# Kernel tuning notes

Measured on AMD Instinct MI355X. Metric: run time of the kernel, lower is better.

## Reference

```python
import jax, jax.numpy as jnp
import numpy as np

N_HEAD = 16

def setup_inputs() -> dict:
    key = jax.random.key(0)
    k1, k2, k3 = jax.random.split(key, 3)
    B, T, C = 4, 2048, 1024
    x = jax.random.normal(k1, (B, T, C), dtype=jnp.float32)
    Wqkv = jax.random.normal(k2, (C, 3 * C), dtype=jnp.float32) * (C ** -0.5)
    bqkv = jnp.zeros((3 * C,), dtype=jnp.float32)
    Wout = jax.random.normal(k3, (C, C), dtype=jnp.float32) * (C ** -0.5)
    bout = jnp.zeros((C,), dtype=jnp.float32)
    return {"x": x, "Wqkv": Wqkv, "bqkv": bqkv, "Wout": Wout, "bout": bout}

def reference(x, Wqkv, bqkv, Wout, bout):
    B, T, C = x.shape
    H = N_HEAD
    hd = C // H
    scale = hd ** -0.5
    qkv = x @ Wqkv + bqkv                      # [B,T,3C]
    q, k, v = jnp.split(qkv, 3, axis=-1)
    # [B,T,C] -> [B,H,T,hd]
    q = q.reshape(B, T, H, hd).transpose(0, 2, 1, 3)
    k = k.reshape(B, T, H, hd).transpose(0, 2, 1, 3)
    v = v.reshape(B, T, H, hd).transpose(0, 2, 1, 3)
    attn = jnp.einsum('bhqd,bhkd->bhqk', q, k) * scale  # [B,H,T,T]
    mask = jnp.tril(jnp.ones((T, T), dtype=bool))
    attn = jnp.where(mask[None, None], attn, -jnp.inf)
    attn = jax.nn.softmax(attn, axis=-1)       # dropout p=0.0 -> identity
    out = jnp.einsum('bhqk,bhkd->bhqd', attn, v)
    out = out.transpose(0, 2, 1, 3).reshape(B, T, C)
    out = out @ Wout + bout
    return (out, k, v)
```

## Files before the change

kernel.cpp:

```cpp
#include <hip/hip_runtime.h>
#include <stdint.h>

typedef short bf16x8 __attribute__((ext_vector_type(8)));
typedef float f32x4 __attribute__((ext_vector_type(4)));

#define MFMA16(A, B, C) __builtin_amdgcn_mfma_f32_16x16x32_bf16((A), (B), (C), 0, 0, 0)

__device__ inline unsigned short f2bf(float x) {
    unsigned int b = __builtin_bit_cast(unsigned int, x);
    b += 0x7fffu + ((b >> 16) & 1u);
    return (unsigned short)(b >> 16);
}
__device__ inline unsigned pack2bf(float x, float y) {
    unsigned a = __builtin_bit_cast(unsigned, x) + 0x8000u;
    unsigned b = __builtin_bit_cast(unsigned, y) + 0x8000u;
    return __builtin_amdgcn_perm(b, a, 0x07060302u);
}

#if __has_builtin(__builtin_amdgcn_exp2f)
#define EXP2(x) __builtin_amdgcn_exp2f(x)
#else
__device__ inline float fast_exp2_(float x) {
    float r;
    asm("v_exp_f32 %0, %1" : "=v"(r) : "v"(x));
    return r;
}
#define EXP2(x) fast_exp2_(x)
#endif

typedef __attribute__((address_space(1))) const void glob_cv;
typedef __attribute__((address_space(3))) void lds_v;
__device__ __forceinline__ void async_copy16(void* lds, const void* g) {
    __builtin_amdgcn_global_load_lds((glob_cv*)g, (lds_v*)lds, 16, 0, 0);
}

__global__ __launch_bounds__(256) void cast_bf16_kernel(const float* __restrict__ in,
                                                        unsigned short* __restrict__ out) {
    size_t g = (size_t)blockIdx.x * 256 + threadIdx.x;
    float4 a = ((const float4*)in)[g * 2 + 0];
    float4 b = ((const float4*)in)[g * 2 + 1];
    union { unsigned short u[8]; uint4 v; } r;
    r.u[0] = f2bf(a.x); r.u[1] = f2bf(a.y); r.u[2] = f2bf(a.z); r.u[3] = f2bf(a.w);
    r.u[4] = f2bf(b.x); r.u[5] = f2bf(b.y); r.u[6] = f2bf(b.z); r.u[7] = f2bf(b.w);
    ((uint4*)out)[g] = r.v;
}

__global__ __launch_bounds__(256) void tcast_kernel(const float* __restrict__ in,
                                                    unsigned short* __restrict__ out,
                                                    int R, int C) {
    __shared__ float tile[32][33];
    int tx = threadIdx.x & 31, ty = threadIdx.x >> 5;
    int c0 = blockIdx.x * 32, r0 = blockIdx.y * 32;
#pragma unroll
    for (int i = 0; i < 4; i++)
        tile[ty + i * 8][tx] = in[(size_t)(r0 + ty + i * 8) * C + c0 + tx];
    __syncthreads();
#pragma unroll
    for (int i = 0; i < 4; i++)
        out[(size_t)(c0 + ty + i * 8) * R + r0 + tx] = f2bf(tile[tx][ty + i * 8]);
}

__global__ __launch_bounds__(256) void tv_kernel(const float* __restrict__ in,
                                                 unsigned short* __restrict__ out) {
    __shared__ float tile[32][33];
    int tx = threadIdx.x & 31, ty = threadIdx.x >> 5;
    int d0 = blockIdx.x * 32, t0 = blockIdx.y * 32, bh = blockIdx.z;
    const float* vin = in + (size_t)bh * 2048 * 64;
    unsigned short* vout = out + (size_t)bh * 64 * 2048;
#pragma unroll
    for (int i = 0; i < 4; i++)
        tile[ty + i * 8][tx] = vin[(size_t)(t0 + ty + i * 8) * 64 + d0 + tx];
    __syncthreads();
#pragma unroll
    for (int i = 0; i < 4; i++)
        vout[(size_t)(d0 + ty + i * 8) * 2048 + t0 + tx] = f2bf(tile[tx][ty + i * 8]);
}

template <int MODE>
__global__ __launch_bounds__(256) void gemm_bt_kernel(
    const unsigned short* __restrict__ A, const unsigned short* __restrict__ Bt,
    const float* __restrict__ bias, int K,
    unsigned short* __restrict__ q_out, float* __restrict__ k_out, float* __restrict__ v_out,
    float* __restrict__ c_out) {
    __shared__ __align__(16) unsigned short As[2 * 128 * 32];
    __shared__ __align__(16) unsigned short Bs[2 * 128 * 32];
    int tid = threadIdx.x;
    int w = tid >> 6, l = tid & 63;
    int quad = l >> 4, cl = l & 15;
    int wm = w & 1, wn = w >> 1;
    int m0 = blockIdx.y * 128, n0 = blockIdx.x * 128;

    f32x4 acc[4][4] = {};

    int srow = w * 16 + (l >> 2);
    int scol = (l & 3) * 8;
    const unsigned short* Ap = A + (size_t)(m0 + srow) * K + scol;
    const unsigned short* Bp = Bt + (size_t)(n0 + srow) * K + scol;

    {
        unsigned short* a0 = &As[w * 512];
        unsigned short* b0 = &Bs[w * 512];
        async_copy16(a0, Ap);
        async_copy16(a0 + 2048, Ap + (size_t)64 * K);
        async_copy16(b0, Bp);
        async_copy16(b0 + 2048, Bp + (size_t)64 * K);
    }

    for (int k0 = 0; k0 < K; k0 += 32) {
        int bo = (k0 >> 5) & 1;
        __syncthreads();
        if (k0 + 32 < K) {
            unsigned short* a0 = &As[(bo ^ 1) * 4096 + w * 512];
            unsigned short* b0 = &Bs[(bo ^ 1) * 4096 + w * 512];
            async_copy16(a0, Ap + k0 + 32);
            async_copy16(a0 + 2048, Ap + (size_t)64 * K + k0 + 32);
            async_copy16(b0, Bp + k0 + 32);
            async_copy16(b0 + 2048, Bp + (size_t)64 * K + k0 + 32);
        }
        bf16x8 af[4], bfr[4];
#pragma unroll
        for (int t = 0; t < 4; t++) {
            af[t]  = *(const bf16x8*)&As[bo * 4096 + (wm * 64 + t * 16 + cl) * 32 + quad * 8];
            bfr[t] = *(const bf16x8*)&Bs[bo * 4096 + (wn * 64 + t * 16 + cl) * 32 + quad * 8];
        }
#pragma unroll
        for (int mt = 0; mt < 4; mt++)
#pragma unroll
            for (int nt = 0; nt < 4; nt++)
                acc[mt][nt] = MFMA16(af[mt], bfr[nt], acc[mt][nt]);
    }

    if (MODE == 0) {
#pragma unroll
        for (int mt = 0; mt < 4; mt++)
#pragma unroll
            for (int nt = 0; nt < 4; nt++) {
                int n = n0 + wn * 64 + nt * 16 + cl;
                float bn = bias[n];
                int sec = n >> 10, cc = n & 1023, h = cc >> 6, d = cc & 63;
#pragma unroll
                for (int r = 0; r < 4; r++) {
                    int m = m0 + wm * 64 + mt * 16 + quad * 4 + r;
                    int b = m >> 11, t = m & 2047;
                    float val = acc[mt][nt][r] + bn;
                    size_t idx = ((size_t)(b * 16 + h) * 2048 + t) * 64 + d;
                    if (sec == 0)      q_out[idx] = f2bf(val * 0.18033688011112042f);
                    else if (sec == 1) k_out[idx] = val;
                    else               v_out[idx] = val;
                }
            }
    } else {
#pragma unroll
        for (int mt = 0; mt < 4; mt++)
#pragma unroll
            for (int nt = 0; nt < 4; nt++) {
                int n = n0 + wn * 64 + nt * 16 + cl;
                float bn = bias[n];
#pragma unroll
                for (int r = 0; r < 4; r++) {
                    int m = m0 + wm * 64 + mt * 16 + quad * 4 + r;
                    c_out[(size_t)m * 1024 + n] = acc[mt][nt][r] + bn;
                }
            }
    }
}

__global__ __launch_bounds__(256) void attn_kernel(
    const unsigned short* __restrict__ Q,
    const float* __restrict__ Kin,
    const unsigned short* __restrict__ Vt,
    unsigned short* __restrict__ Out) {
    __shared__ __align__(16) unsigned short Ks[2 * 64 * 72];
    __shared__ __align__(16) unsigned short Vts[2 * 64 * 64];
    __shared__ __align__(16) unsigned short Ps[128 * 72];
    int tid = threadIdx.x;
    int w = tid >> 6, l = tid & 63;
    int quad = l >> 4, cl = l & 15;
    int cl7 = cl & 7;
    int bh = blockIdx.x;
    int b = bh >> 4, h = bh & 15;
    int qt = 15 - (int)blockIdx.y;
    int qw0 = qt * 128 + w * 32;
    int nkt = 2 * qt + 2;

    int srow = tid >> 2, sch = tid & 3;
    const float* kbase = Kin + ((size_t)bh * 2048 + srow) * 64 + sch * 16;
    unsigned lK = srow * 72 + sch * 16;
    int vrow = 8 * w + (l >> 3);
    int vchk = (l & 7) ^ (l >> 3);
    const unsigned short* vg = Vt + ((size_t)bh * 64 + vrow) * 2048 + vchk * 8;

    const unsigned short* qb = Q + ((size_t)bh * 2048 + qw0 + cl) * 64;
    bf16x8 qf[2][2];
    qf[0][0] = *(const bf16x8*)(qb + quad * 8);
    qf[0][1] = *(const bf16x8*)(qb + 32 + quad * 8);
    qf[1][0] = *(const bf16x8*)(qb + 16 * 64 + quad * 8);
    qf[1][1] = *(const bf16x8*)(qb + 16 * 64 + 32 + quad * 8);

    f32x4 accO[2][4] = {};
    float lloc[2] = {0.f, 0.f};

    float4 kr0, kr1, kr2, kr3;
    {
        const float4* kpp = (const float4*)kbase;
        kr0 = kpp[0]; kr1 = kpp[1]; kr2 = kpp[2]; kr3 = kpp[3];
    }
    {
        unsigned short* vsb = &Vts[w * 512];
        async_copy16(vsb, vg);
        async_copy16(vsb + 2048, vg + (size_t)32 * 2048);
    }

    for (int kt = 0; kt < nkt; ++kt) {
        unsigned bo = (unsigned)(kt & 1);
        uint4 c0, c1;
        c0.x = pack2bf(kr0.x, kr0.y); c0.y = pack2bf(kr0.z, kr0.w);
        c0.z = pack2bf(kr1.x, kr1.y); c0.w = pack2bf(kr1.z, kr1.w);
        c1.x = pack2bf(kr2.x, kr2.y); c1.y = pack2bf(kr2.z, kr2.w);
        c1.z = pack2bf(kr3.x, kr3.y); c1.w = pack2bf(kr3.z, kr3.w);
        *(uint4*)&Ks[bo * 4608 + lK] = c0;
        *(uint4*)&Ks[bo * 4608 + lK + 8] = c1;
        __syncthreads();

        if (kt + 1 < nkt) {
            const float4* kpp = (const float4*)(kbase + (size_t)(kt + 1) * 4096);
            kr0 = kpp[0]; kr1 = kpp[1]; kr2 = kpp[2]; kr3 = kpp[3];
            unsigned short* vsb = &Vts[(bo ^ 1) * 4096 + w * 512];
            async_copy16(vsb, vg + (size_t)(kt + 1) * 64);
            async_copy16(vsb + 2048, vg + (size_t)32 * 2048 + (size_t)(kt + 1) * 64);
        }
        if (kt * 64 > qw0 + 31) continue;

        f32x4 s[2][4];
        __builtin_amdgcn_s_setprio(1);
#pragma unroll
        for (int mt = 0; mt < 4; mt++) {
            bf16x8 kf0 = *(const bf16x8*)&Ks[bo * 4608 + (mt * 16 + cl) * 72 + quad * 8];
            bf16x8 kf1 = *(const bf16x8*)&Ks[bo * 4608 + (mt * 16 + cl) * 72 + 32 + quad * 8];
#pragma unroll
            for (int ng = 0; ng < 2; ng++) {
                f32x4 a = {};
                a = MFMA16(kf0, qf[ng][0], a);
                a = MFMA16(kf1, qf[ng][1], a);
                s[ng][mt] = a;
            }
        }
        __builtin_amdgcn_s_setprio(0);
        if (kt * 64 + 63 > qw0) {
#pragma unroll
            for (int ng = 0; ng < 2; ng++) {
                int qg = qw0 + ng * 16 + cl;
#pragma unroll
                for (int mt = 0; mt < 4; mt++)
#pragma unroll
                    for (int r = 0; r < 4; r++) {
                        int kv = kt * 64 + mt * 16 + quad * 4 + r;
                        if (kv > qg) s[ng][mt][r] = -1e30f;
                    }
            }
        }
        bf16x8 pf[2][2];
#pragma unroll
        for (int ng = 0; ng < 2; ng++) {
            unsigned pbase = (unsigned)(w * 32 + ng * 16 + cl) * 72;
#pragma unroll
            for (int mt = 0; mt < 4; mt++) {
                float e0 = EXP2(s[ng][mt][0]);
                float e1 = EXP2(s[ng][mt][1]);
                float e2 = EXP2(s[ng][mt][2]);
                float e3 = EXP2(s[ng][mt][3]);
                lloc[ng] += (e0 + e1) + (e2 + e3);
                uint2 pv;
                pv.x = pack2bf(e0, e1);
                pv.y = pack2bf(e2, e3);
                *(uint2*)&Ps[pbase + mt * 16 + quad * 4] = pv;
            }
            pf[ng][0] = *(const bf16x8*)&Ps[pbase + quad * 8];
            pf[ng][1] = *(const bf16x8*)&Ps[pbase + 32 + quad * 8];
        }
        __builtin_amdgcn_s_setprio(1);
#pragma unroll
        for (int mt = 0; mt < 4; mt++) {
            int vr = mt * 16 + cl;
            bf16x8 vf0 = *(const bf16x8*)&Vts[bo * 4096 + vr * 64 + (quad ^ cl7) * 8];
            bf16x8 vf1 = *(const bf16x8*)&Vts[bo * 4096 + vr * 64 + ((quad | 4) ^ cl7) * 8];
#pragma unroll
            for (int ng = 0; ng < 2; ng++) {
                accO[ng][mt] = MFMA16(vf0, pf[ng][0], accO[ng][mt]);
                accO[ng][mt] = MFMA16(vf1, pf[ng][1], accO[ng][mt]);
            }
        }
        __builtin_amdgcn_s_setprio(0);
    }

#pragma unroll
    for (int ng = 0; ng < 2; ng++) {
        float lv = lloc[ng];
        lv += __shfl_xor(lv, 16);
        lv += __shfl_xor(lv, 32);
        float inv = 1.0f / lv;
        size_t obase = ((size_t)(b * 2048 + qw0 + ng * 16 + cl)) * 1024 + h * 64;
#pragma unroll
        for (int mt = 0; mt < 4; mt++) {
            uint2 ov;
            ov.x = (unsigned)f2bf(accO[ng][mt][0] * inv) | ((unsigned)f2bf(accO[ng][mt][1] * inv) << 16);
            ov.y = (unsigned)f2bf(accO[ng][mt][2] * inv) | ((unsigned)f2bf(accO[ng][mt][3] * inv) << 16);
            *(uint2*)&Out[obase + mt * 16 + quad * 4] = ov;
        }
    }
}

extern "C" void kernel_launch(void* const* d_in, const int* in_sizes, int n_in,
                              void* d_out, int out_size, void* d_ws, size_t ws_size,
                              hipStream_t stream) {
    const float* x    = (const float*)d_in[0];
    const float* Wqkv = (const float*)d_in[1];
    const float* bqkv = (const float*)d_in[2];
    const float* Wout = (const float*)d_in[3];
    const float* bout = (const float*)d_in[4];

    float* out   = (float*)d_out;
    float* k_out = out + 8388608;
    float* v_out = out + 16777216;

    char* ws = (char*)d_ws;
    unsigned short* xb    = (unsigned short*)(ws);
    unsigned short* WqkvT = (unsigned short*)(ws + 16777216);
    unsigned short* WoutT = (unsigned short*)(ws + 23068672);
    unsigned short* q_ws  = (unsigned short*)(ws + 25165824);
    unsigned short* vT    = (unsigned short*)(ws + 41943040);
    unsigned short* attn  = xb;

    cast_bf16_kernel<<<4096, 256, 0, stream>>>(x, xb);
    tcast_kernel<<<dim3(96, 32), 256, 0, stream>>>(Wqkv, WqkvT, 1024, 3072);
    tcast_kernel<<<dim3(32, 32), 256, 0, stream>>>(Wout, WoutT, 1024, 1024);
    gemm_bt_kernel<0><<<dim3(24, 64), 256, 0, stream>>>(xb, WqkvT, bqkv, 1024,
                                                        q_ws, k_out, v_out, nullptr);
    tv_kernel<<<dim3(2, 64, 64), 256, 0, stream>>>(v_out, vT);
    attn_kernel<<<dim3(64, 16), 256, 0, stream>>>(q_ws, k_out, vT, attn);
    gemm_bt_kernel<1><<<dim3(8, 64), 256, 0, stream>>>(attn, WoutT, bout, 1024,
                                                       nullptr, nullptr, nullptr, out);
}
```

Before: 304.4 us.

## Replace QKV projection GEMM with 256x256-tile, 512-thread pipelined kernel

Adds a dedicated QKV GEMM kernel that computes 256x256 output tiles with 8 waves. It uses a BK=64 double-buffered LDS pipeline fed by async global-to-LDS copies with an XOR-swizzled layout, plus a block-index swizzle to improve L2 reuse. MFMA groups are interleaved with barriers and s_setprio so loads overlap compute, and the larger tiles raise arithmetic intensity over the previous 128x128 kernel. In exchange it uses more registers and LDS (64KB per block), and the hand-written vmcnt/barrier schedule adds risk of correctness or occupancy problems.

```diff
diff --git a/kernel.cpp b/kernel.cpp
--- a/kernel.cpp
+++ b/kernel.cpp
@@ -33,6 +33,9 @@
 __device__ __forceinline__ void async_copy16(void* lds, const void* g) {
     __builtin_amdgcn_global_load_lds((glob_cv*)g, (lds_v*)lds, 16, 0, 0);
 }
+
+#define FENCE asm volatile("" ::: "memory")
+#define SBAR do { FENCE; __builtin_amdgcn_s_barrier(); FENCE; } while (0)
 
 __global__ __launch_bounds__(256) void cast_bf16_kernel(const float* __restrict__ in,
                                                         unsigned short* __restrict__ out) {
@@ -74,6 +77,140 @@
 #pragma unroll
     for (int i = 0; i < 4; i++)
         vout[(size_t)(d0 + ty + i * 8) * 2048 + t0 + tx] = f2bf(tile[tx][ty + i * 8]);
+}
+
+__global__ __launch_bounds__(512, 2) void qkv_gemm256_kernel(
+    const unsigned short* __restrict__ A, const unsigned short* __restrict__ Bt,
+    const float* __restrict__ bias, int K,
+    unsigned short* __restrict__ q_out, float* __restrict__ k_out, float* __restrict__ v_out) {
+    __shared__ __align__(16) unsigned short As[2 * 16384];
+    __shared__ __align__(16) unsigned short Bs[2 * 16384];
+    const int tid = threadIdx.x;
+    const int w = tid >> 6, l = tid & 63;
+    const int quad = l >> 4, cl = l & 15, cl7 = l & 7;
+    const int wm = w & 1, wn = w >> 1;
+
+    int bid = (int)blockIdx.x;
+    int swz = (bid & 7) * 48 + (bid >> 3);
+    const int m0 = (swz / 12) * 256, n0 = (swz % 12) * 256;
+
+    const int srow = w * 8 + (l >> 3);
+    const int schk = (l & 7) ^ ((l >> 3) & 7);
+    const unsigned short* Ag = A + (size_t)(m0 + srow) * K + schk * 8;
+    const unsigned short* Bg = Bt + (size_t)(n0 + srow) * K + schk * 8;
+    const int ldsw = w * 512;
+
+#define STAGE2(base, Gp, h, tk)                                                              \
+    do {                                                                                     \
+        async_copy16((void*)&(base)[(h) * 8192 + ldsw], (Gp) + (size_t)((h) * 128) * K + (tk));          \
+        async_copy16((void*)&(base)[(h) * 8192 + 4096 + ldsw], (Gp) + (size_t)((h) * 128 + 64) * K + (tk)); \
+    } while (0)
+
+    const unsigned aRdBase = wm * 8192 + cl * 64;
+    const unsigned bRdBase = (wn >> 1) * 8192 + (((wn & 1) * 64) + cl) * 64;
+    const unsigned pk0 = ((quad) ^ cl7) * 8;
+    const unsigned pk1 = ((4 + quad) ^ cl7) * 8;
+
+    f32x4 acc[8][4] = {};
+    bf16x8 bf[4][2];
+
+    STAGE2(As, Ag, 0, 0); STAGE2(As, Ag, 1, 0);
+    STAGE2(Bs, Bg, 0, 0); STAGE2(Bs, Bg, 1, 0);
+
+    const int NT = K >> 6;
+
+#define LD_A(ab_, mt_, pk_) (*(const bf16x8*)&As[(ab_) + aRdBase + (mt_) * 1024 + (pk_)])
+
+#define MFMA_PAIR(ma_, mb_, a0_, a1_, b0_, b1_)                    \
+    do {                                                           \
+        __builtin_amdgcn_s_setprio(1);                             \
+        _Pragma("unroll")                                          \
+        for (int nt = 0; nt < 4; nt++) {                           \
+            acc[ma_][nt] = MFMA16(a0_, bf[nt][0], acc[ma_][nt]);   \
+            acc[ma_][nt] = MFMA16(a1_, bf[nt][1], acc[ma_][nt]);   \
+            acc[mb_][nt] = MFMA16(b0_, bf[nt][0], acc[mb_][nt]);   \
+            acc[mb_][nt] = MFMA16(b1_, bf[nt][1], acc[mb_][nt]);   \
+        }                                                          \
+        __builtin_amdgcn_s_setprio(0);                             \
+    } while (0)
+
+#define TILE(kt_, c_)                                                                     \
+    do {                                                                                  \
+        const int ktn = (kt_) + 1;                                                        \
+        const bool hasN = ktn < NT;                                                       \
+        const unsigned ab = (c_) * 16384;                                                 \
+        const unsigned sb = ((c_) ^ 1) * 16384;                                           \
+                \
+        if (hasN) { STAGE2((&As[sb]), Ag, 0, ktn * 64); STAGE2((&Bs[sb]), Bg, 0, ktn * 64); \
+                    asm volatile("s_waitcnt vmcnt(4)" ::: "memory"); }                    \
+        else      { asm volatile("s_waitcnt vmcnt(0)" ::: "memory"); }                    \
+        SBAR;                                           \
+        _Pragma("unroll")                                                                 \
+        for (int nt = 0; nt < 4; nt++) {                                                  \
+            bf[nt][0] = *(const bf16x8*)&Bs[ab + bRdBase + nt * 1024 + pk0];              \
+            bf[nt][1] = *(const bf16x8*)&Bs[ab + bRdBase + nt * 1024 + pk1];              \
+        }                                                                                 \
+        {                                                                                 \
+            bf16x8 a00 = LD_A(ab, 0, pk0), a01 = LD_A(ab, 0, pk1);                        \
+            bf16x8 a10 = LD_A(ab, 1, pk0), a11 = LD_A(ab, 1, pk1);                        \
+            SBAR;                                                                         \
+            MFMA_PAIR(0, 1, a00, a01, a10, a11);                                          \
+            SBAR;                                                                         \
+        }                                                                                 \
+                                                                             \
+        {                                                                                 \
+            bf16x8 a00 = LD_A(ab, 2, pk0), a01 = LD_A(ab, 2, pk1);                        \
+            bf16x8 a10 = LD_A(ab, 3, pk0), a11 = LD_A(ab, 3, pk1);                        \
+            SBAR;                                                                         \
+            MFMA_PAIR(2, 3, a00, a01, a10, a11);                                          \
+            SBAR;                                                                         \
+        }                                                                                 \
+                                                   \
+        {                                                                                 \
+            if (hasN) { STAGE2((&As[sb]), Ag, 1, ktn * 64); STAGE2((&Bs[sb]), Bg, 1, ktn * 64); } \
+            bf16x8 a00 = LD_A(ab, 4, pk0), a01 = LD_A(ab, 4, pk1);                        \
+            bf16x8 a10 = LD_A(ab, 5, pk0), a11 = LD_A(ab, 5, pk1);                        \
+            SBAR;                                                                         \
+            MFMA_PAIR(4, 5, a00, a01, a10, a11);                                          \
+            SBAR;                                                                         \
+        }                                                                                 \
+                                                                             \
+        {                                                                                 \
+            bf16x8 a00 = LD_A(ab, 6, pk0), a01 = LD_A(ab, 6, pk1);                        \
+            bf16x8 a10 = LD_A(ab, 7, pk0), a11 = LD_A(ab, 7, pk1);                        \
+            SBAR;                                                                         \
+            MFMA_PAIR(6, 7, a00, a01, a10, a11);                                          \
+            SBAR;                                                                         \
+        }                                                                                 \
+    } while (0)
+
+    for (int kt = 0; kt < NT; kt += 2) {
+        TILE(kt, 0);
+        TILE(kt + 1, 1);
+    }
+#undef TILE
+#undef MFMA_PAIR
+#undef LD_A
+#undef STAGE2
+
+#pragma unroll
+    for (int mt = 0; mt < 8; mt++)
+#pragma unroll
+        for (int nt = 0; nt < 4; nt++) {
+            int n = n0 + wn * 64 + nt * 16 + cl;
+            float bn = bias[n];
+            int sec = n >> 10, ccc = n & 1023, h = ccc >> 6, d = ccc & 63;
+#pragma unroll
+            for (int r = 0; r < 4; r++) {
+                int m = m0 + wm * 128 + mt * 16 + quad * 4 + r;
+                int b = m >> 11, t = m & 2047;
+                float val = acc[mt][nt][r] + bn;
+                size_t idx = ((size_t)(b * 16 + h) * 2048 + t) * 64 + d;
+                if (sec == 0)      q_out[idx] = f2bf(val * 0.18033688011112042f);
+                else if (sec == 1) k_out[idx] = val;
+                else               v_out[idx] = val;
+            }
+        }
 }
 
 template <int MODE>
@@ -334,8 +471,8 @@
     cast_bf16_kernel<<<4096, 256, 0, stream>>>(x, xb);
     tcast_kernel<<<dim3(96, 32), 256, 0, stream>>>(Wqkv, WqkvT, 1024, 3072);
     tcast_kernel<<<dim3(32, 32), 256, 0, stream>>>(Wout, WoutT, 1024, 1024);
-    gemm_bt_kernel<0><<<dim3(24, 64), 256, 0, stream>>>(xb, WqkvT, bqkv, 1024,
-                                                        q_ws, k_out, v_out, nullptr);
+    qkv_gemm256_kernel<<<384, 512, 0, stream>>>(xb, WqkvT, bqkv, 1024,
+                                                q_ws, k_out, v_out);
     tv_kernel<<<dim3(2, 64, 64), 256, 0, stream>>>(v_out, vT);
     attn_kernel<<<dim3(64, 16), 256, 0, stream>>>(q_ws, k_out, vT, attn);
     gemm_bt_kernel<1><<<dim3(8, 64), 256, 0, stream>>>(attn, WoutT, bout, 1024,
```

Measured after the change: 313.0 us. +2.8%, slower.

## Replace QKV GEMM with 256x256-tile pipelined kernel and fuse V transpose

Applied to the files above, without the earlier changes.

Adds a dedicated QKV projection GEMM using 256x256 tiles, 512 threads, and XOR-swizzled LDS. Loads are async global-to-LDS and double-buffered, with split-phase prefetch, s_setprio around the MFMA bursts, and a block-index swizzle for L2 locality. The epilogue also writes the bf16 transposed V directly, so the separate tv_kernel launch and its re-read of V disappear. The bigger tiles raise register and LDS pressure, and the vT stores are scattered 8-byte writes.

```diff
diff --git a/kernel.cpp b/kernel.cpp
--- a/kernel.cpp
+++ b/kernel.cpp
@@ -33,6 +33,9 @@
 __device__ __forceinline__ void async_copy16(void* lds, const void* g) {
     __builtin_amdgcn_global_load_lds((glob_cv*)g, (lds_v*)lds, 16, 0, 0);
 }
+
+#define FENCE asm volatile("" ::: "memory")
+#define SBAR do { FENCE; __builtin_amdgcn_s_barrier(); FENCE; } while (0)
 
 __global__ __launch_bounds__(256) void cast_bf16_kernel(const float* __restrict__ in,
                                                         unsigned short* __restrict__ out) {
@@ -60,20 +63,128 @@
         out[(size_t)(c0 + ty + i * 8) * R + r0 + tx] = f2bf(tile[tx][ty + i * 8]);
 }
 
-__global__ __launch_bounds__(256) void tv_kernel(const float* __restrict__ in,
-                                                 unsigned short* __restrict__ out) {
-    __shared__ float tile[32][33];
-    int tx = threadIdx.x & 31, ty = threadIdx.x >> 5;
-    int d0 = blockIdx.x * 32, t0 = blockIdx.y * 32, bh = blockIdx.z;
-    const float* vin = in + (size_t)bh * 2048 * 64;
-    unsigned short* vout = out + (size_t)bh * 64 * 2048;
-#pragma unroll
-    for (int i = 0; i < 4; i++)
-        tile[ty + i * 8][tx] = vin[(size_t)(t0 + ty + i * 8) * 64 + d0 + tx];
-    __syncthreads();
-#pragma unroll
-    for (int i = 0; i < 4; i++)
-        vout[(size_t)(d0 + ty + i * 8) * 2048 + t0 + tx] = f2bf(tile[tx][ty + i * 8]);
+__global__ __launch_bounds__(512, 2) void qkv_gemm256_kernel(
+    const unsigned short* __restrict__ A, const unsigned short* __restrict__ Bt,
+    const float* __restrict__ bias, int K,
+    unsigned short* __restrict__ q_out, float* __restrict__ k_out, float* __restrict__ v_out,
+    unsigned short* __restrict__ vT) {
+    __shared__ __align__(16) unsigned short As[2 * 16384];
+    __shared__ __align__(16) unsigned short Bs[2 * 16384];
+    const int tid = threadIdx.x;
+    const int w = tid >> 6, l = tid & 63;
+    const int quad = l >> 4, cl = l & 15, cl7 = l & 7;
+    const int wm = w & 1, wn = w >> 1;
+
+    int bid = (int)blockIdx.x;
+    int swz = (bid & 7) * 48 + (bid >> 3);
+    const int m0 = (swz / 12) * 256, n0 = (swz % 12) * 256;
+
+    const int srow = w * 8 + (l >> 3);
+    const int schk = (l & 7) ^ ((l >> 3) & 7);
+    const unsigned short* Ag = A + (size_t)(m0 + srow) * K + schk * 8;
+    const unsigned short* Bg = Bt + (size_t)(n0 + srow) * K + schk * 8;
+    const int ldsw = w * 512;
+
+#define STAGE2(base, Gp, h, tk)                                                              \
+    do {                                                                                     \
+        async_copy16((void*)&(base)[(h) * 8192 + ldsw], (Gp) + (size_t)((h) * 128) * K + (tk));          \
+        async_copy16((void*)&(base)[(h) * 8192 + 4096 + ldsw], (Gp) + (size_t)((h) * 128 + 64) * K + (tk)); \
+    } while (0)
+
+    const unsigned aRdBase = wm * 8192 + cl * 64;
+    const unsigned bRdBase = (wn >> 1) * 8192 + (((wn & 1) * 64) + cl) * 64;
+    const unsigned pk0 = ((quad) ^ cl7) * 8;
+    const unsigned pk1 = ((4 + quad) ^ cl7) * 8;
+
+    f32x4 acc[8][4] = {};
+
+    STAGE2(As, Ag, 0, 0); STAGE2(As, Ag, 1, 0);
+    STAGE2(Bs, Bg, 0, 0); STAGE2(Bs, Bg, 1, 0);
+
+    const int NT = K >> 6;
+
+#define PHASE(ab_, h_, nn_, PRE)                                                              \
+    do {                                                                                      \
+        bf16x8 af[4][2], bq[2][2];                                                            \
+        _Pragma("unroll")                                                                     \
+        for (int i = 0; i < 4; i++) {                                                         \
+            af[i][0] = *(const bf16x8*)&As[(ab_) + aRdBase + ((h_) * 4 + i) * 1024 + pk0];    \
+            af[i][1] = *(const bf16x8*)&As[(ab_) + aRdBase + ((h_) * 4 + i) * 1024 + pk1];    \
+        }                                                                                     \
+        _Pragma("unroll")                                                                     \
+        for (int j = 0; j < 2; j++) {                                                         \
+            bq[j][0] = *(const bf16x8*)&Bs[(ab_) + bRdBase + ((nn_) * 2 + j) * 1024 + pk0];   \
+            bq[j][1] = *(const bf16x8*)&Bs[(ab_) + bRdBase + ((nn_) * 2 + j) * 1024 + pk1];   \
+        }                                                                                     \
+        PRE;                                                                                  \
+        SBAR;                                                                                 \
+        __builtin_amdgcn_s_setprio(1);                                                        \
+        _Pragma("unroll")                                                                     \
+        for (int i = 0; i < 4; i++)                                                           \
+            _Pragma("unroll")                                                                 \
+            for (int j = 0; j < 2; j++) {                                                     \
+                acc[(h_) * 4 + i][(nn_) * 2 + j] =                                            \
+                    MFMA16(af[i][0], bq[j][0], acc[(h_) * 4 + i][(nn_) * 2 + j]);             \
+                acc[(h_) * 4 + i][(nn_) * 2 + j] =                                            \
+                    MFMA16(af[i][1], bq[j][1], acc[(h_) * 4 + i][(nn_) * 2 + j]);             \
+            }                                                                                 \
+        __builtin_amdgcn_s_setprio(0);                                                        \
+        SBAR;                                                                                 \
+    } while (0)
+
+#define TILE(kt_, c_)                                                                         \
+    do {                                                                                      \
+        const int ktn = (kt_) + 1;                                                            \
+        const bool hasN = ktn < NT;                                                           \
+        const unsigned ab = (c_) * 16384;                                                     \
+        const unsigned sb = ((c_) ^ 1) * 16384;                                               \
+        if (hasN) { STAGE2((&As[sb]), Ag, 0, ktn * 64); STAGE2((&Bs[sb]), Bg, 0, ktn * 64);   \
+                    asm volatile("s_waitcnt vmcnt(4)" ::: "memory"); }                        \
+        else      { asm volatile("s_waitcnt vmcnt(0)" ::: "memory"); }                        \
+        SBAR;                                                            \
+        PHASE(ab, 0, 0, );                                                                    \
+        PHASE(ab, 1, 0,                                                                       \
+              if (hasN) { STAGE2((&As[sb]), Ag, 1, ktn * 64); STAGE2((&Bs[sb]), Bg, 1, ktn * 64); }); \
+        PHASE(ab, 0, 1, );                                                                    \
+        PHASE(ab, 1, 1, );                                                                    \
+    } while (0)
+
+    for (int kt = 0; kt < NT; kt += 2) {
+        TILE(kt, 0);
+        TILE(kt + 1, 1);
+    }
+#undef TILE
+#undef PHASE
+#undef STAGE2
+
+#pragma unroll
+    for (int mt = 0; mt < 8; mt++)
+#pragma unroll
+        for (int nt = 0; nt < 4; nt++) {
+            int n = n0 + wn * 64 + nt * 16 + cl;
+            float bn = bias[n];
+            int sec = n >> 10, ccc = n & 1023, h = ccc >> 6, d = ccc & 63;
+            int mb = m0 + wm * 128 + mt * 16 + quad * 4;
+            int b = mb >> 11, t = mb & 2047;
+            size_t idx0 = ((size_t)(b * 16 + h) * 2048 + t) * 64 + d;
+            if (sec == 0) {
+#pragma unroll
+                for (int r = 0; r < 4; r++)
+                    q_out[idx0 + (size_t)r * 64] = f2bf((acc[mt][nt][r] + bn) * 0.18033688011112042f);
+            } else if (sec == 1) {
+#pragma unroll
+                for (int r = 0; r < 4; r++)
+                    k_out[idx0 + (size_t)r * 64] = acc[mt][nt][r] + bn;
+            } else {
+#pragma unroll
+                for (int r = 0; r < 4; r++)
+                    v_out[idx0 + (size_t)r * 64] = acc[mt][nt][r] + bn;
+                uint2 vv;
+                vv.x = pack2bf(acc[mt][nt][0] + bn, acc[mt][nt][1] + bn);
+                vv.y = pack2bf(acc[mt][nt][2] + bn, acc[mt][nt][3] + bn);
+                *(uint2*)&vT[((size_t)(b * 16 + h) * 64 + d) * 2048 + t] = vv;
+            }
+        }
 }
 
 template <int MODE>
@@ -334,9 +445,8 @@
     cast_bf16_kernel<<<4096, 256, 0, stream>>>(x, xb);
     tcast_kernel<<<dim3(96, 32), 256, 0, stream>>>(Wqkv, WqkvT, 1024, 3072);
     tcast_kernel<<<dim3(32, 32), 256, 0, stream>>>(Wout, WoutT, 1024, 1024);
-    gemm_bt_kernel<0><<<dim3(24, 64), 256, 0, stream>>>(xb, WqkvT, bqkv, 1024,
-                                                        q_ws, k_out, v_out, nullptr);
-    tv_kernel<<<dim3(2, 64, 64), 256, 0, stream>>>(v_out, vT);
+    qkv_gemm256_kernel<<<384, 512, 0, stream>>>(xb, WqkvT, bqkv, 1024,
+                                                q_ws, k_out, v_out, vT);
     attn_kernel<<<dim3(64, 16), 256, 0, stream>>>(q_ws, k_out, vT, attn);
     gemm_bt_kernel<1><<<dim3(8, 64), 256, 0, stream>>>(attn, WoutT, bout, 1024,
                                                        nullptr, nullptr, nullptr, out);
```

Result: slower. 312.7 us (+2.7%).

## Fuse V transpose into QKV GEMM epilogue and unroll K loop by two

Applied to the files above, without the earlier changes.

Removes the separate tv_kernel. The QKV GEMM epilogue now writes the transposed bf16 V directly, packing four consecutive t values into one 8-byte store. This saves a kernel launch and a re-read of the fp32 V tensor. The K loop is manually unrolled over both double buffers so buffer indices are compile-time constants, and launch bounds now request 4 waves per SIMD, which may constrain register allocation. The epilogue also hoists index math out of the per-row loop.

```diff
diff --git a/kernel.cpp b/kernel.cpp
--- a/kernel.cpp
+++ b/kernel.cpp
@@ -60,28 +60,12 @@
         out[(size_t)(c0 + ty + i * 8) * R + r0 + tx] = f2bf(tile[tx][ty + i * 8]);
 }
 
-__global__ __launch_bounds__(256) void tv_kernel(const float* __restrict__ in,
-                                                 unsigned short* __restrict__ out) {
-    __shared__ float tile[32][33];
-    int tx = threadIdx.x & 31, ty = threadIdx.x >> 5;
-    int d0 = blockIdx.x * 32, t0 = blockIdx.y * 32, bh = blockIdx.z;
-    const float* vin = in + (size_t)bh * 2048 * 64;
-    unsigned short* vout = out + (size_t)bh * 64 * 2048;
-#pragma unroll
-    for (int i = 0; i < 4; i++)
-        tile[ty + i * 8][tx] = vin[(size_t)(t0 + ty + i * 8) * 64 + d0 + tx];
-    __syncthreads();
-#pragma unroll
-    for (int i = 0; i < 4; i++)
-        vout[(size_t)(d0 + ty + i * 8) * 2048 + t0 + tx] = f2bf(tile[tx][ty + i * 8]);
-}
-
 template <int MODE>
-__global__ __launch_bounds__(256) void gemm_bt_kernel(
+__global__ __launch_bounds__(256, 4) void gemm_bt_kernel(
     const unsigned short* __restrict__ A, const unsigned short* __restrict__ Bt,
     const float* __restrict__ bias, int K,
     unsigned short* __restrict__ q_out, float* __restrict__ k_out, float* __restrict__ v_out,
-    float* __restrict__ c_out) {
+    unsigned short* __restrict__ vT, float* __restrict__ c_out) {
     __shared__ __align__(16) unsigned short As[2 * 128 * 32];
     __shared__ __align__(16) unsigned short Bs[2 * 128 * 32];
     int tid = threadIdx.x;
@@ -96,39 +80,45 @@
     int scol = (l & 3) * 8;
     const unsigned short* Ap = A + (size_t)(m0 + srow) * K + scol;
     const unsigned short* Bp = Bt + (size_t)(n0 + srow) * K + scol;
-
-    {
-        unsigned short* a0 = &As[w * 512];
-        unsigned short* b0 = &Bs[w * 512];
-        async_copy16(a0, Ap);
-        async_copy16(a0 + 2048, Ap + (size_t)64 * K);
-        async_copy16(b0, Bp);
-        async_copy16(b0 + 2048, Bp + (size_t)64 * K);
-    }
-
-    for (int k0 = 0; k0 < K; k0 += 32) {
-        int bo = (k0 >> 5) & 1;
+    const size_t rstep = (size_t)64 * K;
+
+#define STAGE(bo_, kk_)                                              \
+    do {                                                             \
+        unsigned short* a0 = &As[(bo_) * 4096 + w * 512];            \
+        unsigned short* b0 = &Bs[(bo_) * 4096 + w * 512];            \
+        async_copy16(a0, Ap + (kk_));                                \
+        async_copy16(a0 + 2048, Ap + rstep + (kk_));                 \
+        async_copy16(b0, Bp + (kk_));                                \
+        async_copy16(b0 + 2048, Bp + rstep + (kk_));                 \
+    } while (0)
+
+#define CSTEP(bo_)                                                                            \
+    do {                                                                                      \
+        bf16x8 af[4], bfr[4];                                                                 \
+        _Pragma("unroll")                                                                     \
+        for (int t = 0; t < 4; t++) {                                                         \
+            af[t]  = *(const bf16x8*)&As[(bo_) * 4096 + (wm * 64 + t * 16 + cl) * 32 + quad * 8]; \
+            bfr[t] = *(const bf16x8*)&Bs[(bo_) * 4096 + (wn * 64 + t * 16 + cl) * 32 + quad * 8]; \
+        }                                                                                     \
+        _Pragma("unroll")                                                                     \
+        for (int mt = 0; mt < 4; mt++)                                                        \
+            _Pragma("unroll")                                                                 \
+            for (int nt = 0; nt < 4; nt++)                                                    \
+                acc[mt][nt] = MFMA16(af[mt], bfr[nt], acc[mt][nt]);                           \
+    } while (0)
+
+    STAGE(0, 0);
+
+    for (int k0 = 0; k0 < K; k0 += 64) {
         __syncthreads();
-        if (k0 + 32 < K) {
-            unsigned short* a0 = &As[(bo ^ 1) * 4096 + w * 512];
-            unsigned short* b0 = &Bs[(bo ^ 1) * 4096 + w * 512];
-            async_copy16(a0, Ap + k0 + 32);
-            async_copy16(a0 + 2048, Ap + (size_t)64 * K + k0 + 32);
-            async_copy16(b0, Bp + k0 + 32);
-            async_copy16(b0 + 2048, Bp + (size_t)64 * K + k0 + 32);
-        }
-        bf16x8 af[4], bfr[4];
-#pragma unroll
-        for (int t = 0; t < 4; t++) {
-            af[t]  = *(const bf16x8*)&As[bo * 4096 + (wm * 64 + t * 16 + cl) * 32 + quad * 8];
-            bfr[t] = *(const bf16x8*)&Bs[bo * 4096 + (wn * 64 + t * 16 + cl) * 32 + quad * 8];
-        }
-#pragma unroll
-        for (int mt = 0; mt < 4; mt++)
-#pragma unroll
-            for (int nt = 0; nt < 4; nt++)
-                acc[mt][nt] = MFMA16(af[mt], bfr[nt], acc[mt][nt]);
-    }
+        if (k0 + 32 < K) STAGE(1, k0 + 32);
+        CSTEP(0);
+        __syncthreads();
+        if (k0 + 64 < K) STAGE(0, k0 + 64);
+        CSTEP(1);
+    }
+#undef CSTEP
+#undef STAGE
 
     if (MODE == 0) {
 #pragma unroll
@@ -138,15 +128,25 @@
                 int n = n0 + wn * 64 + nt * 16 + cl;
                 float bn = bias[n];
                 int sec = n >> 10, cc = n & 1023, h = cc >> 6, d = cc & 63;
-#pragma unroll
-                for (int r = 0; r < 4; r++) {
-                    int m = m0 + wm * 64 + mt * 16 + quad * 4 + r;
-                    int b = m >> 11, t = m & 2047;
-                    float val = acc[mt][nt][r] + bn;
-                    size_t idx = ((size_t)(b * 16 + h) * 2048 + t) * 64 + d;
-                    if (sec == 0)      q_out[idx] = f2bf(val * 0.18033688011112042f);
-                    else if (sec == 1) k_out[idx] = val;
-                    else               v_out[idx] = val;
+                int mb = m0 + wm * 64 + mt * 16 + quad * 4;
+                int b = mb >> 11, t = mb & 2047;
+                size_t idx0 = ((size_t)(b * 16 + h) * 2048 + t) * 64 + d;
+                if (sec == 0) {
+#pragma unroll
+                    for (int r = 0; r < 4; r++)
+                        q_out[idx0 + (size_t)r * 64] = f2bf((acc[mt][nt][r] + bn) * 0.18033688011112042f);
+                } else if (sec == 1) {
+#pragma unroll
+                    for (int r = 0; r < 4; r++)
+                        k_out[idx0 + (size_t)r * 64] = acc[mt][nt][r] + bn;
+                } else {
+#pragma unroll
+                    for (int r = 0; r < 4; r++)
+                        v_out[idx0 + (size_t)r * 64] = acc[mt][nt][r] + bn;
+                    uint2 vv;
+                    vv.x = pack2bf(acc[mt][nt][0] + bn, acc[mt][nt][1] + bn);
+                    vv.y = pack2bf(acc[mt][nt][2] + bn, acc[mt][nt][3] + bn);
+                    *(uint2*)&vT[((size_t)(b * 16 + h) * 64 + d) * 2048 + t] = vv;
                 }
             }
     } else {
@@ -335,9 +335,8 @@
     tcast_kernel<<<dim3(96, 32), 256, 0, stream>>>(Wqkv, WqkvT, 1024, 3072);
     tcast_kernel<<<dim3(32, 32), 256, 0, stream>>>(Wout, WoutT, 1024, 1024);
     gemm_bt_kernel<0><<<dim3(24, 64), 256, 0, stream>>>(xb, WqkvT, bqkv, 1024,
-                                                        q_ws, k_out, v_out, nullptr);
-    tv_kernel<<<dim3(2, 64, 64), 256, 0, stream>>>(v_out, vT);
+                                                        q_ws, k_out, v_out, vT, nullptr);
     attn_kernel<<<dim3(64, 16), 256, 0, stream>>>(q_ws, k_out, vT, attn);
     gemm_bt_kernel<1><<<dim3(8, 64), 256, 0, stream>>>(attn, WoutT, bout, 1024,
-                                                       nullptr, nullptr, nullptr, out);
-}
+                                                       nullptr, nullptr, nullptr, nullptr, out);
+}
```

Result: faster. 292.5 us (-3.9%).
